# Performance work log

Hardware: AMD Instinct MI355X
Metric: run time of the kernel (lower is better)

Reference implementation:

```python
import jax, jax.numpy as jnp
import numpy as np
import math

B, S, D, H = 2, 2048, 512, 8  # batch, seq, d_hidden (= per-head dim here), n_heads


def _rope(x):
    # x: [B, H, S, D]; standard interleaved RoPE with base 10000
    b, h, s, d = x.shape
    inv_freq = 1.0 / (10000.0 ** (jnp.arange(0, d, 2, dtype=jnp.float32) / d))  # [d/2]
    ang = jnp.arange(s, dtype=jnp.float32)[:, None] * inv_freq[None, :]          # [S, d/2]
    cos, sin = jnp.cos(ang), jnp.sin(ang)
    x1, x2 = x[..., 0::2], x[..., 1::2]
    r1 = x1 * cos - x2 * sin
    r2 = x1 * sin + x2 * cos
    return jnp.stack([r1, r2], axis=-1).reshape(b, h, s, d).astype(x.dtype)


def setup_inputs() -> dict:
    key = jax.random.key(0)
    kq, k1, k2, k3, k4 = jax.random.split(key, 5)
    std = 0.02
    return {
        "q": jax.random.normal(kq, (B, S, D), dtype=jnp.float32),
        "W_q": jax.random.normal(k1, (H, D, D), dtype=jnp.float32) * std,
        "W_k": jax.random.normal(k2, (H, D, D), dtype=jnp.float32) * std,
        "W_v": jax.random.normal(k3, (H, D, D), dtype=jnp.float32) * std,
        "W_o": jax.random.normal(k4, (H * D, D), dtype=jnp.float32) * std,
    }


def reference(q, W_q, W_k, W_v, W_o):
    b, s, d = q.shape
    h = W_q.shape[0]
    scale = 1.0 / math.sqrt(d)
    qh = jnp.einsum('bsz,hzd->bhsd', q, W_q)
    kh = jnp.einsum('bsz,hzd->bhsd', q, W_k)
    vh = jnp.einsum('bsz,hzd->bhsd', q, W_v)
    qh = _rope(qh)
    kh = _rope(kh)
    scores = jnp.einsum('bhqd,bhkd->bhqk', qh, kh) * scale
    causal = jnp.triu(jnp.ones((s, s), dtype=bool), k=1)  # True above diagonal
    scores = jnp.where(causal, -jnp.inf, scores)
    probs = jax.nn.softmax(scores, axis=-1)  # dropout is identity in eval
    # NOTE: faithful to the original (transposed) einsum: contracts over the
    # query index z of probs with the sequence index z of v.
    out = jnp.einsum('bhzs,bhzd->bhsd', probs, vh)
    out = out.transpose(0, 2, 1, 3).reshape(b, s, h * d)
    return jnp.einsum('bsz,zd->bsd', out, W_o)
```

## Files before the change

kernel.cpp:

```cpp
#include <hip/hip_runtime.h>
#include <hip/hip_bf16.h>
#include <math.h>
#include <stdint.h>

#define BB 2
#define SS 2048
#define DD 512
#define HH 8
#define NTOK (BB*SS)
#define NQKV (3*HH*DD)
#define BHD  (HH*DD)
#define NBH  (BB*HH)
#define NTILE 136

typedef __attribute__((ext_vector_type(8))) short short8v;
typedef __attribute__((ext_vector_type(4))) float floatx4;

__device__ __forceinline__ unsigned short f2bf(float f) {
  unsigned int u = __builtin_bit_cast(unsigned int, f);
  u = (u + 0x7FFFu + ((u >> 16) & 1u)) >> 16;
  return (unsigned short)u;
}
__device__ __forceinline__ float bf2f(unsigned short s) {
  unsigned int u = ((unsigned int)s) << 16;
  return __builtin_bit_cast(float, u);
}
__device__ __forceinline__ void async16(const void* g, void* l) {
  __builtin_amdgcn_global_load_lds(
      (const __attribute__((address_space(1))) unsigned int*)g,
      (__attribute__((address_space(3))) unsigned int*)l, 16, 0, 0);
}

__global__ void k_convert_q(const float* __restrict__ q, unsigned short* __restrict__ qbf) {
  int i = (blockIdx.x * 256 + threadIdx.x) * 4;
  const float4 v = *(const float4*)&q[i];
  ushort4 o;
  o.x = f2bf(v.x); o.y = f2bf(v.y); o.z = f2bf(v.z); o.w = f2bf(v.w);
  *(ushort4*)&qbf[i] = o;
}

__global__ void k_rope_tab(float* __restrict__ rope) {
  const int idx = blockIdx.x * 256 + threadIdx.x;
  const int dp = idx >> 11, s = idx & 2047;
  const float inv = exp2f(-13.287712379549449f * (1.0f/256.0f) * (float)dp);
  float sn, cs;
  __sincosf((float)s * inv, &sn, &cs);
  rope[(size_t)idx * 2]     = cs;
  rope[(size_t)idx * 2 + 1] = sn;
}

__global__ void k_prep_w(const float* __restrict__ Wq, const float* __restrict__ Wk,
                         const float* __restrict__ Wv, const float* __restrict__ Wo,
                         unsigned short* __restrict__ Wcat, unsigned short* __restrict__ Wot) {
  __shared__ float t[32][33];
  const int z = blockIdx.z;
  const float* in; unsigned short* out; int inLD, outLD;
  float sc = 1.0f;
  if (z < 24) {
    int tsel = z / 8, h = z % 8;
    const float* w = (tsel == 0) ? Wq : (tsel == 1) ? Wk : Wv;
    if (tsel == 0) sc = 0.044194173824159216f;
    in = w + (size_t)h * DD * DD;
    out = Wcat + ((size_t)tsel * BHD + (size_t)h * DD) * DD;
    inLD = DD; outLD = DD;
  } else {
    int k = z - 24;
    in = Wo + (size_t)k * DD * DD;
    out = Wot + (size_t)k * DD;
    inLD = DD; outLD = BHD;
  }
  const int tx = threadIdx.x, ty = threadIdx.y;
  const int bx = blockIdx.x * 32, by = blockIdx.y * 32;
  for (int kk = 0; kk < 4; ++kk)
    t[ty + 8*kk][tx] = in[(size_t)(by + ty + 8*kk) * inLD + bx + tx];
  __syncthreads();
  for (int kk = 0; kk < 4; ++kk)
    out[(size_t)(bx + ty + 8*kk) * outLD + by + tx] = f2bf(t[tx][ty + 8*kk] * sc);
}

__global__ __launch_bounds__(256, 2)
void k_qkv(const unsigned short* __restrict__ Abf, const unsigned short* __restrict__ Bt,
           const float* __restrict__ rope,
           unsigned short* __restrict__ Qr, unsigned short* __restrict__ Kr,
           unsigned short* __restrict__ Vt) {
  __shared__ short As[128*32];
  __shared__ short Bs[256*32];
  const int tid = threadIdx.x;
  const int m0 = blockIdx.x * 128;
  const int n0 = blockIdx.y * 256;
  const int wave = tid >> 6, lane = tid & 63, qd = lane >> 4, c = lane & 15;
  const int wm = (wave >> 1) * 64, wn = (wave & 1) * 128;
  floatx4 acc[4][8] = {};
  const int e0 = tid * 8;
  const int r0 = e0 >> 5, c0 = e0 & 31;
  for (int k0 = 0; k0 < 512; k0 += 32) {
    __syncthreads();
    async16(&Abf[(size_t)(m0 + r0      ) * 512 + k0 + c0], &As[e0]);
    async16(&Abf[(size_t)(m0 + r0 +  64) * 512 + k0 + c0], &As[e0 + 2048]);
    async16(&Bt [(size_t)(n0 + r0      ) * 512 + k0 + c0], &Bs[e0]);
    async16(&Bt [(size_t)(n0 + r0 +  64) * 512 + k0 + c0], &Bs[e0 + 2048]);
    async16(&Bt [(size_t)(n0 + r0 + 128) * 512 + k0 + c0], &Bs[e0 + 4096]);
    async16(&Bt [(size_t)(n0 + r0 + 192) * 512 + k0 + c0], &Bs[e0 + 6144]);
    __syncthreads();
    short8v a[4], bfr[8];
    for (int mt = 0; mt < 4; ++mt) a[mt]   = *(const short8v*)&As[(wm + mt*16 + c)*32 + qd*8];
    for (int nt = 0; nt < 8; ++nt) bfr[nt] = *(const short8v*)&Bs[(wn + nt*16 + c)*32 + qd*8];
    for (int mt = 0; mt < 4; ++mt)
      for (int nt = 0; nt < 8; ++nt)
        acc[mt][nt] = __builtin_amdgcn_mfma_f32_16x16x32_bf16(a[mt], bfr[nt], acc[mt][nt], 0, 0, 0);
  }
  const int tsel = n0 >> 12;
  const int h = (n0 >> 9) & 7;
  const int bat = m0 >> 11;
  const int bh = bat * HH + h;
  const int dloc = (n0 & 511) + wn;
  if (tsel < 2) {
    unsigned short* dst = (tsel == 0) ? Qr : Kr;
    for (int nt = 0; nt < 8; ++nt) {
      const int d = dloc + nt*16 + c;
      const unsigned int sgn = (d & 1) ? 0u : 0x80000000u;
      const size_t rb = (size_t)(d >> 1) * (SS * 2);
      for (int mt = 0; mt < 4; ++mt) {
        const int mrow = (m0 & 2047) + wm + mt*16 + qd*4;
        const float4 t0 = *(const float4*)&rope[rb + (size_t)mrow * 2];
        const float4 t1 = *(const float4*)&rope[rb + (size_t)mrow * 2 + 4];
        const float cs[4] = {t0.x, t0.z, t1.x, t1.z};
        const float sn[4] = {t0.y, t0.w, t1.y, t1.w};
        for (int r = 0; r < 4; ++r) {
          const float v = acc[mt][nt][r];
          float p = __shfl_xor(v, 1, 64);
          p = __builtin_bit_cast(float, __builtin_bit_cast(unsigned int, p) ^ sgn);
          const float res = fmaf(p, sn[r], v * cs[r]);
          dst[((size_t)bh * SS + mrow + r) * DD + d] = f2bf(res);
        }
      }
    }
  } else {
    for (int nt = 0; nt < 8; ++nt) {
      const int d = dloc + nt*16 + c;
      const size_t vbase = ((size_t)bh * DD + d) * SS;
      for (int mt = 0; mt < 4; ++mt) {
        const int s = (m0 & 2047) + wm + mt*16 + qd*4;
        ushort4 u;
        u.x = f2bf(acc[mt][nt][0]); u.y = f2bf(acc[mt][nt][1]);
        u.z = f2bf(acc[mt][nt][2]); u.w = f2bf(acc[mt][nt][3]);
        *(ushort4*)&Vt[vbase + s] = u;
      }
    }
  }
}

__global__ __launch_bounds__(256)
void k_scores(const unsigned short* __restrict__ Qr, const unsigned short* __restrict__ Kr,
              unsigned short* __restrict__ Eg, float* __restrict__ lsum) {
  __shared__ short UN[17408];
  short* As0 = UN;
  short* As1 = UN + 4096;
  short* Bs0 = UN + 8192;
  short* Bs1 = UN + 12288;
  unsigned short* ET = (unsigned short*)UN;
  const int tid = threadIdx.x;
  const int bh = blockIdx.y;
  const int t = blockIdx.x;
  int zb = 0;
  while (((zb + 1) * (zb + 2)) / 2 <= t) ++zb;
  const int st = t - (zb * (zb + 1)) / 2;
  const int z0 = zb * 128, s0 = st * 128;
  const int wave = tid >> 6, lane = tid & 63, qd = lane >> 4, c = lane & 15;
  const int wm = (wave >> 1) * 64, wn = (wave & 1) * 64;
  const size_t qb = (size_t)bh * SS * DD;
  floatx4 acc[4][4] = {};
  const int e0 = tid * 8, e1 = e0 + 2048;
  const int r0 = e0 >> 5, c0 = e0 & 31, r1 = e1 >> 5, c1 = e1 & 31;
  for (int k0 = 0; k0 < 512; k0 += 64) {
    __syncthreads();
    async16(&Qr[qb + (size_t)(z0 + r0) * 512 + k0      + c0], &As0[e0]);
    async16(&Qr[qb + (size_t)(z0 + r1) * 512 + k0      + c1], &As0[e1]);
    async16(&Qr[qb + (size_t)(z0 + r0) * 512 + k0 + 32 + c0], &As1[e0]);
    async16(&Qr[qb + (size_t)(z0 + r1) * 512 + k0 + 32 + c1], &As1[e1]);
    async16(&Kr[qb + (size_t)(s0 + r0) * 512 + k0      + c0], &Bs0[e0]);
    async16(&Kr[qb + (size_t)(s0 + r1) * 512 + k0      + c1], &Bs0[e1]);
    async16(&Kr[qb + (size_t)(s0 + r0) * 512 + k0 + 32 + c0], &Bs1[e0]);
    async16(&Kr[qb + (size_t)(s0 + r1) * 512 + k0 + 32 + c1], &Bs1[e1]);
    __syncthreads();
    for (int kc = 0; kc < 2; ++kc) {
      const short* Asp = kc ? As1 : As0;
      const short* Bsp = kc ? Bs1 : Bs0;
      short8v a[4], bfr[4];
      for (int mt = 0; mt < 4; ++mt) a[mt]   = *(const short8v*)&Asp[(wm + mt*16 + c)*32 + qd*8];
      for (int nt = 0; nt < 4; ++nt) bfr[nt] = *(const short8v*)&Bsp[(wn + nt*16 + c)*32 + qd*8];
      for (int mt = 0; mt < 4; ++mt)
        for (int nt = 0; nt < 4; ++nt)
          acc[mt][nt] = __builtin_amdgcn_mfma_f32_16x16x32_bf16(a[mt], bfr[nt], acc[mt][nt], 0, 0, 0);
    }
  }
  const bool diag = (st == zb);
  for (int mt = 0; mt < 4; ++mt) {
    const int zl = wm + mt*16 + qd*4;
    float rs[4] = {0.f, 0.f, 0.f, 0.f};
    for (int nt = 0; nt < 4; ++nt) {
      const int sl = wn + nt*16 + c;
      for (int r = 0; r < 4; ++r) {
        float ev = __expf(acc[mt][nt][r]);
        if (diag && (sl > zl + r)) ev = 0.f;
        acc[mt][nt][r] = ev;
        rs[r] += ev;
      }
    }
    for (int off = 1; off < 16; off <<= 1)
      for (int r = 0; r < 4; ++r) rs[r] += __shfl_xor(rs[r], off, 64);
    if (c == 0)
      for (int r = 0; r < 4; ++r)
        atomicAdd(&lsum[(size_t)bh * SS + z0 + zl + r], rs[r]);
  }
  __syncthreads();
  for (int mt = 0; mt < 4; ++mt) {
    const int zl = wm + mt*16 + qd*4;
    for (int nt = 0; nt < 4; ++nt) {
      const int sl = wn + nt*16 + c;
      ushort4 u;
      u.x = f2bf(acc[mt][nt][0]); u.y = f2bf(acc[mt][nt][1]);
      u.z = f2bf(acc[mt][nt][2]); u.w = f2bf(acc[mt][nt][3]);
      *(ushort4*)&ET[sl * 136 + zl] = u;
    }
  }
  __syncthreads();
  const size_t tb = ((size_t)bh * NTILE + t) * 16384;
  for (int it = 0; it < 8; ++it) {
    const int e = it * 2048 + tid * 8;
    const int row = e >> 7, col = e & 127;
    *(short8v*)&Eg[tb + row * 128 + col] = *(const short8v*)&ET[row * 136 + col];
  }
}

__global__ void k_vscale(unsigned short* __restrict__ Vt, const float* __restrict__ lsum) {
  const int idx = (blockIdx.x * 256 + threadIdx.x) * 8;
  const int z = idx & (SS - 1);
  const int bh = idx >> 20;
  short8v v = *(const short8v*)&Vt[idx];
  const float* lp = &lsum[(size_t)bh * SS + z];
  short8v o;
  for (int i = 0; i < 8; ++i)
    o[i] = (short)f2bf(bf2f((unsigned short)v[i]) / lp[i]);
  *(short8v*)&Vt[idx] = o;
}

__global__ __launch_bounds__(256)
void k_pv(const unsigned short* __restrict__ Eg, const unsigned short* __restrict__ Vs,
          unsigned short* __restrict__ Ocat) {
  __shared__ short Vl[2][128*32];
  __shared__ short El[2][128*32];
  const int tid = threadIdx.x;
  const int d0 = blockIdx.x * 128;
  const int pr = blockIdx.y;
  const int bh = blockIdx.z;
  const int bat = bh >> 3, h = bh & 7;
  const int wave = tid >> 6, lane = tid & 63, qd = lane >> 4, c = lane & 15;
  const int wm = (wave >> 1) * 64, wn = (wave & 1) * 64;
  const size_t vbb = (size_t)bh * DD * SS;
  const int e = tid * 8;
  for (int sel = 0; sel < 2; ++sel) {
    const int st = sel ? (15 - pr) : pr;
    const int s0 = st * 128;
    floatx4 acc[4][4] = {};
    for (int zb = st; zb < 16; ++zb) {
      const size_t tb = ((size_t)bh * NTILE + (zb * (zb + 1)) / 2 + st) * 16384;
      for (int half = 0; half < 2; ++half) {
        const int zbase = zb * 128 + half * 64;
        __syncthreads();
        for (int i = 0; i < 4; ++i) {
          const int ee = e + i * 2048;
          const int kc = ee >> 12, row = (ee >> 5) & 127, col = ee & 31;
          async16(&Vs[vbb + (size_t)(d0 + row) * SS + zbase + kc * 32 + col], &Vl[kc][row * 32 + col]);
        }
        for (int i = 0; i < 4; ++i) {
          const int ee = e + i * 2048;
          const int kc = ee >> 12, row = (ee >> 5) & 127, col = ee & 31;
          async16(&Eg[tb + (size_t)row * 128 + half * 64 + kc * 32 + col], &El[kc][row * 32 + col]);
        }
        __syncthreads();
        for (int kc = 0; kc < 2; ++kc) {
          short8v a[4], b[4];
          for (int dt = 0; dt < 4; ++dt) a[dt] = *(const short8v*)&Vl[kc][(wm + dt*16 + c)*32 + qd*8];
          for (int nt = 0; nt < 4; ++nt) b[nt] = *(const short8v*)&El[kc][(wn + nt*16 + c)*32 + qd*8];
          for (int dt = 0; dt < 4; ++dt)
            for (int nt = 0; nt < 4; ++nt)
              acc[dt][nt] = __builtin_amdgcn_mfma_f32_16x16x32_bf16(a[dt], b[nt], acc[dt][nt], 0, 0, 0);
        }
      }
    }
    for (int nt = 0; nt < 4; ++nt) {
      const int sg = s0 + wn + nt*16 + c;
      const size_t ob = ((size_t)(bat * SS + sg)) * BHD + (size_t)h * DD + d0;
      for (int dt = 0; dt < 4; ++dt) {
        const int dloc = wm + dt*16 + qd*4;
        ushort4 u;
        u.x = f2bf(acc[dt][nt][0]); u.y = f2bf(acc[dt][nt][1]);
        u.z = f2bf(acc[dt][nt][2]); u.w = f2bf(acc[dt][nt][3]);
        *(ushort4*)&Ocat[ob + dloc] = u;
      }
    }
  }
}

__global__ __launch_bounds__(256)
void k_oproj(const unsigned short* __restrict__ Ocat, const unsigned short* __restrict__ Wot,
             float* __restrict__ out) {
  __shared__ short As[2][128*32];
  __shared__ short Bs[2][128*32];
  const int tid = threadIdx.x;
  const int m0 = blockIdx.x * 128;
  const int n0 = blockIdx.y * 128;
  const int ks = blockIdx.z * 1024;
  const int wave = tid >> 6, lane = tid & 63, qd = lane >> 4, c = lane & 15;
  const int wm = (wave >> 1) * 64, wn = (wave & 1) * 64;
  floatx4 acc[4][4] = {};
  const int e0 = tid * 8, e1 = e0 + 2048;
  const int r0 = e0 >> 5, c0 = e0 & 31, r1 = e1 >> 5, c1 = e1 & 31;
  for (int k0 = ks; k0 < ks + 1024; k0 += 64) {
    __syncthreads();
    for (int kc = 0; kc < 2; ++kc) {
      const int kk = k0 + kc * 32;
      async16(&Ocat[(size_t)(m0 + r0) * BHD + kk + c0], &As[kc][e0]);
      async16(&Ocat[(size_t)(m0 + r1) * BHD + kk + c1], &As[kc][e1]);
      async16(&Wot [(size_t)(n0 + r0) * BHD + kk + c0], &Bs[kc][e0]);
      async16(&Wot [(size_t)(n0 + r1) * BHD + kk + c1], &Bs[kc][e1]);
    }
    __syncthreads();
    for (int kc = 0; kc < 2; ++kc) {
      short8v a[4], b[4];
      for (int mt = 0; mt < 4; ++mt) a[mt] = *(const short8v*)&As[kc][(wm + mt*16 + c)*32 + qd*8];
      for (int nt = 0; nt < 4; ++nt) b[nt] = *(const short8v*)&Bs[kc][(wn + nt*16 + c)*32 + qd*8];
      for (int mt = 0; mt < 4; ++mt)
        for (int nt = 0; nt < 4; ++nt)
          acc[mt][nt] = __builtin_amdgcn_mfma_f32_16x16x32_bf16(a[mt], b[nt], acc[mt][nt], 0, 0, 0);
    }
  }
  for (int mt = 0; mt < 4; ++mt) {
    const int m = m0 + wm + mt*16 + qd*4;
    for (int nt = 0; nt < 4; ++nt) {
      const int n = n0 + wn + nt*16 + c;
      for (int r = 0; r < 4; ++r)
        atomicAdd(&out[(size_t)(m + r) * DD + n], acc[mt][nt][r]);
    }
  }
}

extern "C" void kernel_launch(void* const* d_in, const int* in_sizes, int n_in,
                              void* d_out, int out_size, void* d_ws, size_t ws_size,
                              hipStream_t stream) {
  const float* q  = (const float*)d_in[0];
  const float* Wq = (const float*)d_in[1];
  const float* Wk = (const float*)d_in[2];
  const float* Wv = (const float*)d_in[3];
  const float* Wo = (const float*)d_in[4];

  char* base = (char*)d_ws;
  unsigned short* Eg   = (unsigned short*)base;
  unsigned short* qbf  = (unsigned short*)base;
  unsigned short* Wcat = (unsigned short*)(base + 4194304);
  float*          rope = (float*)(base + 16777216);
  char* p = base + 71303168;
  unsigned short* Wot  = (unsigned short*)p; p += 4194304;
  unsigned short* Qr   = (unsigned short*)p;
  unsigned short* Ocat = (unsigned short*)p; p += 33554432;
  unsigned short* Kr   = (unsigned short*)p; p += 33554432;
  unsigned short* Vt   = (unsigned short*)p; p += 33554432;
  float*          lsum = (float*)p;

  hipMemsetAsync(lsum, 0, (size_t)NBH * SS * 4, stream);
  hipMemsetAsync(d_out, 0, (size_t)NTOK * DD * 4, stream);

  k_convert_q<<<NTOK*DD/1024, 256, 0, stream>>>(q, qbf);
  k_rope_tab<<<SS*256/256, 256, 0, stream>>>(rope);
  k_prep_w<<<dim3(16,16,32), dim3(32,8), 0, stream>>>(Wq, Wk, Wv, Wo, Wcat, Wot);
  k_qkv<<<dim3(32,48), 256, 0, stream>>>(qbf, Wcat, rope, Qr, Kr, Vt);
  k_scores<<<dim3(NTILE,16), 256, 0, stream>>>(Qr, Kr, Eg, lsum);
  k_vscale<<<NBH*DD*SS/(256*8), 256, 0, stream>>>(Vt, lsum);
  k_pv<<<dim3(4,8,16), 256, 0, stream>>>(Eg, Vt, Ocat);
  k_oproj<<<dim3(32,4,4), 256, 0, stream>>>(Ocat, Wot, (float*)d_out);
}
```

Measured before the change: 400.0 us.

## Share V tiles across paired query tiles in PV; stage RoPE Q/K stores through LDS

```diff
diff --git a/kernel.cpp b/kernel.cpp
--- a/kernel.cpp
+++ b/kernel.cpp
@@ -83,8 +83,10 @@
            const float* __restrict__ rope,
            unsigned short* __restrict__ Qr, unsigned short* __restrict__ Kr,
            unsigned short* __restrict__ Vt) {
-  __shared__ short As[128*32];
-  __shared__ short Bs[256*32];
+  __shared__ short SMEM[12288];
+  short* As = SMEM;
+  short* Bs = SMEM + 4096;
+  unsigned short* CS = (unsigned short*)SMEM;
   const int tid = threadIdx.x;
   const int m0 = blockIdx.x * 128;
   const int n0 = blockIdx.y * 256;
@@ -114,24 +116,42 @@
   const int bat = m0 >> 11;
   const int bh = bat * HH + h;
   const int dloc = (n0 & 511) + wn;
+  const int mybase = m0 & 2047;
   if (tsel < 2) {
     unsigned short* dst = (tsel == 0) ? Qr : Kr;
-    for (int nt = 0; nt < 8; ++nt) {
-      const int d = dloc + nt*16 + c;
-      const unsigned int sgn = (d & 1) ? 0u : 0x80000000u;
-      const size_t rb = (size_t)(d >> 1) * (SS * 2);
-      for (int mt = 0; mt < 4; ++mt) {
-        const int mrow = (m0 & 2047) + wm + mt*16 + qd*4;
-        const float4 t0 = *(const float4*)&rope[rb + (size_t)mrow * 2];
-        const float4 t1 = *(const float4*)&rope[rb + (size_t)mrow * 2 + 4];
-        const float cs[4] = {t0.x, t0.z, t1.x, t1.z};
-        const float sn[4] = {t0.y, t0.w, t1.y, t1.w};
-        for (int r = 0; r < 4; ++r) {
-          const float v = acc[mt][nt][r];
-          float p = __shfl_xor(v, 1, 64);
-          p = __builtin_bit_cast(float, __builtin_bit_cast(unsigned int, p) ^ sgn);
-          const float res = fmaf(p, sn[r], v * cs[r]);
-          dst[((size_t)bh * SS + mrow + r) * DD + d] = f2bf(res);
+    for (int wnsel = 0; wnsel < 2; ++wnsel) {
+      for (int half = 0; half < 2; ++half) {
+        __syncthreads();
+        if ((wave & 1) == wnsel) {
+          for (int nt4 = 0; nt4 < 4; ++nt4) {
+            const int nt = half * 4 + nt4;
+            const int d = dloc + nt * 16 + c;
+            const int dcol = nt4 * 16 + c;
+            const unsigned int sgn = (d & 1) ? 0u : 0x80000000u;
+            const size_t rb = (size_t)(d >> 1) * (SS * 2);
+            for (int mt = 0; mt < 4; ++mt) {
+              const int lrow = wm + mt * 16 + qd * 4;
+              const int mrow = mybase + lrow;
+              const float4 t0 = *(const float4*)&rope[rb + (size_t)mrow * 2];
+              const float4 t1 = *(const float4*)&rope[rb + (size_t)mrow * 2 + 4];
+              const float cs4[4] = {t0.x, t0.z, t1.x, t1.z};
+              const float sn4[4] = {t0.y, t0.w, t1.y, t1.w};
+              for (int r = 0; r < 4; ++r) {
+                const float v = acc[mt][nt][r];
+                float pp = __shfl_xor(v, 1, 64);
+                pp = __builtin_bit_cast(float, __builtin_bit_cast(unsigned int, pp) ^ sgn);
+                CS[(lrow + r) * 68 + dcol] = f2bf(fmaf(pp, sn4[r], v * cs4[r]));
+              }
+            }
+          }
+        }
+        __syncthreads();
+        const int colb = (tid & 7) * 8;
+        const int dbase = (n0 & 511) + wnsel * 128 + half * 64;
+        for (int rr = 0; rr < 4; ++rr) {
+          const int row = rr * 32 + (tid >> 3);
+          short8v vv = *(const short8v*)&CS[row * 68 + colb];
+          *(short8v*)&dst[((size_t)bh * SS + mybase + row) * DD + dbase + colb] = vv;
         }
       }
     }
@@ -140,7 +160,7 @@
       const int d = dloc + nt*16 + c;
       const size_t vbase = ((size_t)bh * DD + d) * SS;
       for (int mt = 0; mt < 4; ++mt) {
-        const int s = (m0 & 2047) + wm + mt*16 + qd*4;
+        const int s = mybase + wm + mt*16 + qd*4;
         ushort4 u;
         u.x = f2bf(acc[mt][nt][0]); u.y = f2bf(acc[mt][nt][1]);
         u.z = f2bf(acc[mt][nt][2]); u.w = f2bf(acc[mt][nt][3]);
@@ -249,46 +269,65 @@
 void k_pv(const unsigned short* __restrict__ Eg, const unsigned short* __restrict__ Vs,
           unsigned short* __restrict__ Ocat) {
   __shared__ short Vl[2][128*32];
-  __shared__ short El[2][128*32];
+  __shared__ short ElA[2][128*32];
+  __shared__ short ElB[2][128*32];
   const int tid = threadIdx.x;
   const int d0 = blockIdx.x * 128;
   const int pr = blockIdx.y;
   const int bh = blockIdx.z;
+  const int stA = pr, stB = 15 - pr;
   const int bat = bh >> 3, h = bh & 7;
   const int wave = tid >> 6, lane = tid & 63, qd = lane >> 4, c = lane & 15;
   const int wm = (wave >> 1) * 64, wn = (wave & 1) * 64;
   const size_t vbb = (size_t)bh * DD * SS;
   const int e = tid * 8;
-  for (int sel = 0; sel < 2; ++sel) {
-    const int st = sel ? (15 - pr) : pr;
-    const int s0 = st * 128;
-    floatx4 acc[4][4] = {};
-    for (int zb = st; zb < 16; ++zb) {
-      const size_t tb = ((size_t)bh * NTILE + (zb * (zb + 1)) / 2 + st) * 16384;
-      for (int half = 0; half < 2; ++half) {
-        const int zbase = zb * 128 + half * 64;
-        __syncthreads();
+  floatx4 accA[4][4] = {};
+  floatx4 accB[4][4] = {};
+  for (int zb = stA; zb < 16; ++zb) {
+    const bool actB = (zb >= stB);
+    const size_t tri = (size_t)bh * NTILE + (zb * (zb + 1)) / 2;
+    const size_t tbA = (tri + stA) * 16384;
+    const size_t tbB = (tri + stB) * 16384;
+    for (int half = 0; half < 2; ++half) {
+      const int zbase = zb * 128 + half * 64;
+      __syncthreads();
+      for (int i = 0; i < 4; ++i) {
+        const int ee = e + i * 2048;
+        const int kc = ee >> 12, row = (ee >> 5) & 127, col = ee & 31;
+        async16(&Vs[vbb + (size_t)(d0 + row) * SS + zbase + kc * 32 + col], &Vl[kc][row * 32 + col]);
+      }
+      for (int i = 0; i < 4; ++i) {
+        const int ee = e + i * 2048;
+        const int kc = ee >> 12, row = (ee >> 5) & 127, col = ee & 31;
+        async16(&Eg[tbA + (size_t)row * 128 + half * 64 + kc * 32 + col], &ElA[kc][row * 32 + col]);
+      }
+      if (actB)
         for (int i = 0; i < 4; ++i) {
           const int ee = e + i * 2048;
           const int kc = ee >> 12, row = (ee >> 5) & 127, col = ee & 31;
-          async16(&Vs[vbb + (size_t)(d0 + row) * SS + zbase + kc * 32 + col], &Vl[kc][row * 32 + col]);
+          async16(&Eg[tbB + (size_t)row * 128 + half * 64 + kc * 32 + col], &ElB[kc][row * 32 + col]);
         }
-        for (int i = 0; i < 4; ++i) {
-          const int ee = e + i * 2048;
-          const int kc = ee >> 12, row = (ee >> 5) & 127, col = ee & 31;
-          async16(&Eg[tb + (size_t)row * 128 + half * 64 + kc * 32 + col], &El[kc][row * 32 + col]);
-        }
-        __syncthreads();
-        for (int kc = 0; kc < 2; ++kc) {
-          short8v a[4], b[4];
-          for (int dt = 0; dt < 4; ++dt) a[dt] = *(const short8v*)&Vl[kc][(wm + dt*16 + c)*32 + qd*8];
-          for (int nt = 0; nt < 4; ++nt) b[nt] = *(const short8v*)&El[kc][(wn + nt*16 + c)*32 + qd*8];
+      __syncthreads();
+      for (int kc = 0; kc < 2; ++kc) {
+        short8v a[4], bA[4];
+        for (int dt = 0; dt < 4; ++dt) a[dt] = *(const short8v*)&Vl[kc][(wm + dt*16 + c)*32 + qd*8];
+        for (int nt = 0; nt < 4; ++nt) bA[nt] = *(const short8v*)&ElA[kc][(wn + nt*16 + c)*32 + qd*8];
+        for (int dt = 0; dt < 4; ++dt)
+          for (int nt = 0; nt < 4; ++nt)
+            accA[dt][nt] = __builtin_amdgcn_mfma_f32_16x16x32_bf16(a[dt], bA[nt], accA[dt][nt], 0, 0, 0);
+        if (actB) {
+          short8v bB[4];
+          for (int nt = 0; nt < 4; ++nt) bB[nt] = *(const short8v*)&ElB[kc][(wn + nt*16 + c)*32 + qd*8];
           for (int dt = 0; dt < 4; ++dt)
             for (int nt = 0; nt < 4; ++nt)
-              acc[dt][nt] = __builtin_amdgcn_mfma_f32_16x16x32_bf16(a[dt], b[nt], acc[dt][nt], 0, 0, 0);
+              accB[dt][nt] = __builtin_amdgcn_mfma_f32_16x16x32_bf16(a[dt], bB[nt], accB[dt][nt], 0, 0, 0);
         }
       }
     }
+  }
+  for (int sel = 0; sel < 2; ++sel) {
+    const int s0 = (sel ? stB : stA) * 128;
+    floatx4 (&acc)[4][4] = sel ? accB : accA;
     for (int nt = 0; nt < 4; ++nt) {
       const int sg = s0 + wn + nt*16 + c;
       const size_t ob = ((size_t)(bat * SS + sg)) * BHD + (size_t)h * DD + d0;
```

Result: slower. 441.2 us (+10.3%).

## Share V tile loads across both paired query tiles in PV kernel

Applied to the files above, without the earlier changes.

```diff
diff --git a/kernel.cpp b/kernel.cpp
--- a/kernel.cpp
+++ b/kernel.cpp
@@ -249,46 +249,65 @@
 void k_pv(const unsigned short* __restrict__ Eg, const unsigned short* __restrict__ Vs,
           unsigned short* __restrict__ Ocat) {
   __shared__ short Vl[2][128*32];
-  __shared__ short El[2][128*32];
+  __shared__ short ElA[2][128*32];
+  __shared__ short ElB[2][128*32];
   const int tid = threadIdx.x;
   const int d0 = blockIdx.x * 128;
   const int pr = blockIdx.y;
   const int bh = blockIdx.z;
+  const int stA = pr, stB = 15 - pr;
   const int bat = bh >> 3, h = bh & 7;
   const int wave = tid >> 6, lane = tid & 63, qd = lane >> 4, c = lane & 15;
   const int wm = (wave >> 1) * 64, wn = (wave & 1) * 64;
   const size_t vbb = (size_t)bh * DD * SS;
   const int e = tid * 8;
-  for (int sel = 0; sel < 2; ++sel) {
-    const int st = sel ? (15 - pr) : pr;
-    const int s0 = st * 128;
-    floatx4 acc[4][4] = {};
-    for (int zb = st; zb < 16; ++zb) {
-      const size_t tb = ((size_t)bh * NTILE + (zb * (zb + 1)) / 2 + st) * 16384;
-      for (int half = 0; half < 2; ++half) {
-        const int zbase = zb * 128 + half * 64;
-        __syncthreads();
+  floatx4 accA[4][4] = {};
+  floatx4 accB[4][4] = {};
+  for (int zb = stA; zb < 16; ++zb) {
+    const bool actB = (zb >= stB);
+    const size_t tri = (size_t)bh * NTILE + (zb * (zb + 1)) / 2;
+    const size_t tbA = (tri + stA) * 16384;
+    const size_t tbB = (tri + stB) * 16384;
+    for (int half = 0; half < 2; ++half) {
+      const int zbase = zb * 128 + half * 64;
+      __syncthreads();
+      for (int i = 0; i < 4; ++i) {
+        const int ee = e + i * 2048;
+        const int kc = ee >> 12, row = (ee >> 5) & 127, col = ee & 31;
+        async16(&Vs[vbb + (size_t)(d0 + row) * SS + zbase + kc * 32 + col], &Vl[kc][row * 32 + col]);
+      }
+      for (int i = 0; i < 4; ++i) {
+        const int ee = e + i * 2048;
+        const int kc = ee >> 12, row = (ee >> 5) & 127, col = ee & 31;
+        async16(&Eg[tbA + (size_t)row * 128 + half * 64 + kc * 32 + col], &ElA[kc][row * 32 + col]);
+      }
+      if (actB)
         for (int i = 0; i < 4; ++i) {
           const int ee = e + i * 2048;
           const int kc = ee >> 12, row = (ee >> 5) & 127, col = ee & 31;
-          async16(&Vs[vbb + (size_t)(d0 + row) * SS + zbase + kc * 32 + col], &Vl[kc][row * 32 + col]);
+          async16(&Eg[tbB + (size_t)row * 128 + half * 64 + kc * 32 + col], &ElB[kc][row * 32 + col]);
         }
-        for (int i = 0; i < 4; ++i) {
-          const int ee = e + i * 2048;
-          const int kc = ee >> 12, row = (ee >> 5) & 127, col = ee & 31;
-          async16(&Eg[tb + (size_t)row * 128 + half * 64 + kc * 32 + col], &El[kc][row * 32 + col]);
-        }
-        __syncthreads();
-        for (int kc = 0; kc < 2; ++kc) {
-          short8v a[4], b[4];
-          for (int dt = 0; dt < 4; ++dt) a[dt] = *(const short8v*)&Vl[kc][(wm + dt*16 + c)*32 + qd*8];
-          for (int nt = 0; nt < 4; ++nt) b[nt] = *(const short8v*)&El[kc][(wn + nt*16 + c)*32 + qd*8];
+      __syncthreads();
+      for (int kc = 0; kc < 2; ++kc) {
+        short8v a[4], bA[4];
+        for (int dt = 0; dt < 4; ++dt) a[dt] = *(const short8v*)&Vl[kc][(wm + dt*16 + c)*32 + qd*8];
+        for (int nt = 0; nt < 4; ++nt) bA[nt] = *(const short8v*)&ElA[kc][(wn + nt*16 + c)*32 + qd*8];
+        for (int dt = 0; dt < 4; ++dt)
+          for (int nt = 0; nt < 4; ++nt)
+            accA[dt][nt] = __builtin_amdgcn_mfma_f32_16x16x32_bf16(a[dt], bA[nt], accA[dt][nt], 0, 0, 0);
+        if (actB) {
+          short8v bB[4];
+          for (int nt = 0; nt < 4; ++nt) bB[nt] = *(const short8v*)&ElB[kc][(wn + nt*16 + c)*32 + qd*8];
           for (int dt = 0; dt < 4; ++dt)
             for (int nt = 0; nt < 4; ++nt)
-              acc[dt][nt] = __builtin_amdgcn_mfma_f32_16x16x32_bf16(a[dt], b[nt], acc[dt][nt], 0, 0, 0);
+              accB[dt][nt] = __builtin_amdgcn_mfma_f32_16x16x32_bf16(a[dt], bB[nt], accB[dt][nt], 0, 0, 0);
         }
       }
     }
+  }
+  for (int sel = 0; sel < 2; ++sel) {
+    const int s0 = (sel ? stB : stA) * 128;
+    floatx4 (&acc)[4][4] = sel ? accB : accA;
     for (int nt = 0; nt < 4; ++nt) {
       const int sg = s0 + wn + nt*16 + c;
       const size_t ob = ((size_t)(bat * SS + sg)) * BHD + (size_t)h * DD + d0;
```

Result: no change. 405.7 us (+1.4%).
